# Optimization experiments

Measured on AMD Instinct MI355X. Metric: run time of the kernel, lower is better.

The kernel has to match this reference:

```python
import jax, jax.numpy as jnp
import numpy as np

N = 8192        # number of samples
D = 128         # embedding dim
K = 20          # n_neighbors (sklearn kneighbors includes self when querying the fitted set)
C = 10          # num classes
THRESH = -0.5   # INFLO score threshold (module default)
EPS = 1e-10


def setup_inputs() -> dict:
    key = jax.random.key(0)
    k1, k2 = jax.random.split(key)
    return {
        "embeddings": jax.random.normal(k1, (N, D), dtype=jnp.float32),
        "logits": jax.random.normal(k2, (N, C), dtype=jnp.float32),
    }


def _inflo_scores(x):
    # pairwise euclidean distances (p=2), [N, N]
    sq = jnp.sum(x * x, axis=-1)
    d2 = sq[:, None] + sq[None, :] - 2.0 * (x @ x.T)
    dist = jnp.sqrt(jnp.maximum(d2, 0.0))
    # k nearest neighbors per row (self included, distance 0) == sklearn kneighbors on fitted set
    neg_knn_d, knn_idx = jax.lax.top_k(-dist, K)
    knn_d = -neg_knn_d                                   # [N, K]
    # local density: 1 / (mean kNN distance)
    density = 1.0 / (jnp.mean(knn_d, axis=-1) + EPS)     # [N]
    # kNN membership mask: Kmask[i, j] = j in knn(i)
    rows = jnp.arange(N)[:, None]
    kmask = jnp.zeros((N, N), dtype=bool).at[rows, knn_idx].set(True)
    # influence space = knn(i) UNION rnn(i), where rnn(i) = {j : i in knn(j)}
    infl = kmask | kmask.T                               # set union (deduplicated)
    inflf = infl.astype(x.dtype)
    # average influence density over the (non-empty: self always included) influence set
    avg = (inflf @ density) / jnp.maximum(jnp.sum(inflf, axis=-1), 1.0)
    # inflo score (negated, as in the module)
    return -(density / (avg + EPS))


def reference(embeddings, logits):
    scores = _inflo_scores(embeddings)
    ood_flags = scores < THRESH
    cls_preds = jnp.where(ood_flags, -1, jnp.argmax(logits, axis=-1))
    return scores, ood_flags, cls_preds
```

## Files before the change

### kernel.cpp

```cpp
#include <hip/hip_runtime.h>
#include <cstdint>
#include <cstddef>

#define N 8192
#define D 128
#define KNN 20
#define NC 10
#define CAPB 448
#define SLOTS 16
#define ZTH 2.1f
#define NW (N / 32)
constexpr float EPS = 1e-10f;

typedef __attribute__((ext_vector_type(8))) short short8;
typedef __attribute__((ext_vector_type(4))) float f32x4;

__device__ inline unsigned short f32_to_bf16_rne(float x) {
    unsigned u = __float_as_uint(x);
    unsigned r = u + 0x7FFFu + ((u >> 16) & 1u);
    return (unsigned short)(r >> 16);
}
__device__ inline float bf16_to_f32(unsigned short h) {
    return __uint_as_float((unsigned)h << 16);
}
__device__ inline unsigned long long pack_key(float d, int j) {
    return ((unsigned long long)__float_as_uint(d) << 14) | (unsigned long long)(j + 1);
}

__global__ void k_sqnorm(const float* __restrict__ X, float* __restrict__ sq) {
    int row = blockIdx.x;
    int lane = threadIdx.x;
    const float2* X2 = (const float2*)(X + (size_t)row * D);
    float2 a = X2[lane];
    float s = a.x * a.x + a.y * a.y;
    #pragma unroll
    for (int off = 32; off; off >>= 1) s += __shfl_down(s, off, 64);
    if (lane == 0) sq[row] = s;
}

__global__ void k_split(const float* __restrict__ X, unsigned short* __restrict__ Xhi,
                        unsigned short* __restrict__ Xlo) {
    int i = blockIdx.x * 256 + threadIdx.x;
    const float4* X4 = (const float4*)X;
    float4 x = X4[i];
    unsigned short h[4], l[4];
    float xs[4] = {x.x, x.y, x.z, x.w};
    #pragma unroll
    for (int q = 0; q < 4; ++q) {
        h[q] = f32_to_bf16_rne(xs[q]);
        float hf = bf16_to_f32(h[q]);
        l[q] = f32_to_bf16_rne(xs[q] - hf);
    }
    *(ushort4*)&Xhi[(size_t)i * 4] = make_ushort4(h[0], h[1], h[2], h[3]);
    *(ushort4*)&Xlo[(size_t)i * 4] = make_ushort4(l[0], l[1], l[2], l[3]);
}

__global__ __launch_bounds__(128) void k_moments(const float* __restrict__ X,
                                                 const float* __restrict__ sq,
                                                 float* __restrict__ m1,
                                                 float* __restrict__ msc) {
    int b = blockIdx.x, t = threadIdx.x;
    int r0 = b * 64;
    float s1 = 0.f;
    for (int r = 0; r < 64; ++r) s1 += X[(size_t)(r0 + r) * D + t];
    atomicAdd(&m1[t], s1);
    if (t < 64) {
        float s = sq[r0 + t];
        float ss1 = s, ss2 = s * s;
        #pragma unroll
        for (int off = 32; off; off >>= 1) {
            ss1 += __shfl_down(ss1, off, 64);
            ss2 += __shfl_down(ss2, off, 64);
        }
        if (t == 0) { atomicAdd(&msc[0], ss1); atomicAdd(&msc[1], ss2); }
    }
}

__global__ void k_thresh(const float* __restrict__ X, const float* __restrict__ sq,
                         const float* __restrict__ m1, const float* __restrict__ msc,
                         float* __restrict__ T) {
    int row = blockIdx.x, lane = threadIdx.x;
    const float2* X2 = (const float2*)(X + (size_t)row * D);
    const float2* M2 = (const float2*)m1;
    float2 a = X2[lane], m = M2[lane];
    float dotp = a.x * m.x + a.y * m.y;
    #pragma unroll
    for (int off = 32; off; off >>= 1) dotp += __shfl_down(dotp, off, 64);
    if (lane == 0) {
        const float invN = 1.f / N;
        float Esq   = msc[0] * invN;
        float Esq2  = msc[1] * invN;
        float varSq = fmaxf(Esq2 - Esq * Esq, 0.f);
        float s  = sq[row];
        float mu = s + Esq - 2.f * dotp * invN;
        float var = varSq + 4.f * s;
        T[row] = mu - ZTH * sqrtf(var);
    }
}

#define ASTRIDE 40
struct StageS {
    unsigned short Ahi[128 * ASTRIDE];
    unsigned short Alo[128 * ASTRIDE];
    unsigned short Bhi[128 * ASTRIDE];
    unsigned short Blo[128 * ASTRIDE];
};
struct EpiS {
    unsigned long long slots[128 * SLOTS];
    unsigned rc[128];
    unsigned rbase[128];
};
__global__ __launch_bounds__(256, 3) void k_distf2(
        const unsigned short* __restrict__ Xhi, const unsigned short* __restrict__ Xlo,
        const float* __restrict__ sqn, const float* __restrict__ Tthr,
        int* __restrict__ cnt, unsigned long long* __restrict__ rowbuf, int capb) {
    __shared__ alignas(16) union { StageS s; EpiS e; } U;

    const int t    = threadIdx.x;
    const int lane = t & 63;
    const int w    = t >> 6;
    const int wr   = w >> 1;
    const int wc   = w & 1;
    const int lrow = lane & 15;
    const int lkg  = lane >> 4;

    const int rowTile = blockIdx.y * 128;
    const int colTile = blockIdx.x * 128;

    f32x4 acc[4][4];
    #pragma unroll
    for (int i = 0; i < 4; ++i)
        #pragma unroll
        for (int j = 0; j < 4; ++j) acc[i][j] = (f32x4){0.f, 0.f, 0.f, 0.f};

    for (int kc = 0; kc < 4; ++kc) {
        const int kb = kc * 32;
        __syncthreads();
        #pragma unroll
        for (int p = 0; p < 2; ++p) {
            int u = t + 256 * p, r = u >> 2, c = u & 3;
            size_t g = (size_t)(rowTile + r) * 128 + kb + c * 8;
            *(uint4*)&U.s.Ahi[r * ASTRIDE + c * 8] = *(const uint4*)&Xhi[g];
            *(uint4*)&U.s.Alo[r * ASTRIDE + c * 8] = *(const uint4*)&Xlo[g];
        }
        #pragma unroll
        for (int p = 0; p < 2; ++p) {
            int u = t + 256 * p, r = u >> 2, c = u & 3;
            size_t g = (size_t)(colTile + r) * 128 + kb + c * 8;
            *(uint4*)&U.s.Bhi[r * ASTRIDE + c * 8] = *(const uint4*)&Xhi[g];
            *(uint4*)&U.s.Blo[r * ASTRIDE + c * 8] = *(const uint4*)&Xlo[g];
        }
        __syncthreads();

        short8 a[4], b[4];
        #pragma unroll
        for (int i = 0; i < 4; ++i)
            a[i] = *(const short8*)&U.s.Ahi[(wr * 64 + 16 * i + lrow) * ASTRIDE + lkg * 8];
        #pragma unroll
        for (int j = 0; j < 4; ++j)
            b[j] = *(const short8*)&U.s.Bhi[(wc * 64 + 16 * j + lrow) * ASTRIDE + lkg * 8];
        #pragma unroll
        for (int i = 0; i < 4; ++i)
            #pragma unroll
            for (int j = 0; j < 4; ++j)
                acc[i][j] = __builtin_amdgcn_mfma_f32_16x16x32_bf16(a[i], b[j], acc[i][j], 0, 0, 0);
        #pragma unroll
        for (int j = 0; j < 4; ++j)
            b[j] = *(const short8*)&U.s.Blo[(wc * 64 + 16 * j + lrow) * ASTRIDE + lkg * 8];
        #pragma unroll
        for (int i = 0; i < 4; ++i)
            #pragma unroll
            for (int j = 0; j < 4; ++j)
                acc[i][j] = __builtin_amdgcn_mfma_f32_16x16x32_bf16(a[i], b[j], acc[i][j], 0, 0, 0);
        #pragma unroll
        for (int i = 0; i < 4; ++i)
            a[i] = *(const short8*)&U.s.Alo[(wr * 64 + 16 * i + lrow) * ASTRIDE + lkg * 8];
        #pragma unroll
        for (int j = 0; j < 4; ++j)
            b[j] = *(const short8*)&U.s.Bhi[(wc * 64 + 16 * j + lrow) * ASTRIDE + lkg * 8];
        #pragma unroll
        for (int i = 0; i < 4; ++i)
            #pragma unroll
            for (int j = 0; j < 4; ++j)
                acc[i][j] = __builtin_amdgcn_mfma_f32_16x16x32_bf16(a[i], b[j], acc[i][j], 0, 0, 0);
    }

    __syncthreads();
    if (t < 128) U.e.rc[t] = 0;
    __syncthreads();

    float sqb[4]; int gcol[4];
    #pragma unroll
    for (int j = 0; j < 4; ++j) {
        gcol[j] = colTile + wc * 64 + 16 * j + lrow;
        sqb[j]  = sqn[gcol[j]];
    }
    #pragma unroll
    for (int i = 0; i < 4; ++i) {
        int lr0 = wr * 64 + 16 * i + lkg * 4;
        #pragma unroll
        for (int q = 0; q < 4; ++q) {
            int lr = lr0 + q;
            float sa = sqn[rowTile + lr];
            float Ti = Tthr[rowTile + lr];
            #pragma unroll
            for (int j = 0; j < 4; ++j) {
                float d = fmaxf(fmaf(-2.f, acc[i][j][q], sa + sqb[j]), 0.f);
                if (d < Ti) {
                    unsigned o = atomicAdd(&U.e.rc[lr], 1u);
                    if (o < SLOTS) U.e.slots[lr * SLOTS + o] = pack_key(d, gcol[j]);
                }
            }
        }
    }
    __syncthreads();
    if (t < 128) {
        unsigned nr = U.e.rc[t];
        if (nr > SLOTS) {
            atomicAdd(&cnt[rowTile + t], capb + 1);
            U.e.rbase[t] = 0xFFFFFFFFu;
        } else if (nr > 0) {
            U.e.rbase[t] = (unsigned)atomicAdd(&cnt[rowTile + t], (int)nr);
        } else {
            U.e.rbase[t] = 0;
        }
    }
    __syncthreads();
    #pragma unroll
    for (int it = 0; it < (128 * SLOTS) / 256; ++it) {
        int idx = t + 256 * it;
        int r = idx / SLOTS, s = idx % SLOTS;
        unsigned nr = U.e.rc[r], base = U.e.rbase[r];
        if ((unsigned)s < min(nr, (unsigned)SLOTS) && base != 0xFFFFFFFFu) {
            unsigned pos = base + (unsigned)s;
            if (pos < (unsigned)capb)
                rowbuf[(size_t)(rowTile + r) * capb + pos] = U.e.slots[idx];
        }
    }
}

__global__ __launch_bounds__(64) void k_sel2(const unsigned long long* __restrict__ rowbuf,
                                             const int* __restrict__ cnt,
                                             int* __restrict__ knn_idx,
                                             float* __restrict__ density,
                                             int* __restrict__ flagged,
                                             int* __restrict__ nflag, int capb) {
    int row = blockIdx.x, t = threadIdx.x;
    int n = cnt[row];
    if (n < KNN || n > capb) {
        if (t == 0) { int p = atomicAdd(nflag, 1); flagged[p] = row; }
        return;
    }
    const unsigned long long* rb = rowbuf + (size_t)row * capb;
    unsigned long long v[7];
    #pragma unroll
    for (int k = 0; k < 7; ++k) { int idx = t + 64 * k; v[k] = idx < n ? rb[idx] : ~0ull; }
    unsigned long long last = 0ull;
    float sumd = 0.f;
    for (int r = 0; r < KNN; ++r) {
        unsigned long long m = ~0ull;
        #pragma unroll
        for (int k = 0; k < 7; ++k) if (v[k] > last && v[k] < m) m = v[k];
        #pragma unroll
        for (int off = 32; off; off >>= 1) {
            unsigned long long o = __shfl_down(m, off, 64);
            if (o < m) m = o;
        }
        m = __shfl(m, 0, 64);
        last = m;
        if (t == 0) {
            int j = (int)(m & 16383ull) - 1;
            if (j < 0) j = 0; if (j >= N) j = N - 1;
            knn_idx[(size_t)row * KNN + r] = j;
            sumd += sqrtf(__uint_as_float((unsigned)(m >> 14)));
        }
    }
    if (t == 0) density[row] = 1.f / (sumd * (1.f / KNN) + EPS);
}

__global__ __launch_bounds__(256) void k_fallback(const float* __restrict__ X,
                                                  const float* __restrict__ sq,
                                                  const int* __restrict__ nflag,
                                                  const int* __restrict__ flagged,
                                                  int* __restrict__ knn_idx,
                                                  float* __restrict__ density) {
    __shared__ float xr[D];
    __shared__ unsigned long long red[256];
    int t = threadIdx.x;
    int nf = *nflag;
    for (int f = blockIdx.x; f < nf; f += gridDim.x) {
        int row = flagged[f];
        __syncthreads();
        if (t < D) xr[t] = X[(size_t)row * D + t];
        __syncthreads();
        float sqr = sq[row];
        unsigned long long keys[32];
        for (int i = 0; i < 32; ++i) {
            int col = t + 256 * i;
            const float4* cp = (const float4*)(X + (size_t)col * D);
            float dot = 0.f;
            #pragma unroll
            for (int d4 = 0; d4 < 32; ++d4) {
                float4 c = cp[d4];
                float4 x = *(const float4*)&xr[d4 * 4];
                dot = fmaf(c.x, x.x, dot); dot = fmaf(c.y, x.y, dot);
                dot = fmaf(c.z, x.z, dot); dot = fmaf(c.w, x.w, dot);
            }
            float d2v = fmaxf(sqr + sq[col] - 2.f * dot, 0.f);
            keys[i] = pack_key(d2v, col);
        }
        unsigned long long last = 0ull;
        float sumd = 0.f;
        for (int r = 0; r < KNN; ++r) {
            unsigned long long m = ~0ull;
            #pragma unroll
            for (int i = 0; i < 32; ++i) if (keys[i] > last && keys[i] < m) m = keys[i];
            red[t] = m; __syncthreads();
            for (int s = 128; s; s >>= 1) {
                if (t < s && red[t + s] < red[t]) red[t] = red[t + s];
                __syncthreads();
            }
            m = red[0]; __syncthreads();
            last = m;
            if (t == 0) {
                int j = (int)(m & 16383ull) - 1;
                if (j < 0) j = 0; if (j >= N) j = N - 1;
                knn_idx[(size_t)row * KNN + r] = j;
                sumd += sqrtf(__uint_as_float((unsigned)(m >> 14)));
            }
        }
        if (t == 0) density[row] = 1.f / (sumd * (1.f / KNN) + EPS);
    }
}

__global__ void k_setbits(const int* __restrict__ knn_idx, unsigned* __restrict__ bits) {
    int p = blockIdx.x * 256 + threadIdx.x;
    if (p >= N * KNN) return;
    int i = p / KNN;
    int j = knn_idx[p];
    atomicOr(&bits[(size_t)i * NW + (j >> 5)], 1u << (j & 31));
}

__global__ void k_rowsum(const int* __restrict__ knn_idx, const float* __restrict__ density,
                         float* __restrict__ numer, float* __restrict__ cntb) {
    int i = blockIdx.x * 256 + threadIdx.x;
    if (i >= N) return;
    const int* ki = knn_idx + (size_t)i * KNN;
    float s = 0.f;
    #pragma unroll
    for (int m = 0; m < KNN; ++m) s += density[ki[m]];
    numer[i] = s;
    cntb[i] = (float)KNN;
}

__global__ void k_rev(const int* __restrict__ knn_idx, const float* __restrict__ density,
                      const unsigned* __restrict__ bits,
                      float* __restrict__ numer, float* __restrict__ cntb) {
    int p = blockIdx.x * 256 + threadIdx.x;
    if (p >= N * KNN) return;
    int i = p / KNN;
    int j = knn_idx[p];
    unsigned wd = bits[(size_t)j * NW + (i >> 5)];
    if (!(wd & (1u << (i & 31)))) {
        atomicAdd(&numer[j], density[i]);
        atomicAdd(&cntb[j], 1.f);
    }
}

__global__ void k_final(const float* __restrict__ density, const float* __restrict__ numer,
                        const float* __restrict__ cntb, const float* __restrict__ logits,
                        float* __restrict__ out) {
    int i = blockIdx.x * 256 + threadIdx.x;
    if (i >= N) return;
    float c     = fmaxf(cntb[i], 1.f);
    float avg   = numer[i] / c;
    float score = -(density[i] / (avg + EPS));
    out[i] = score;
    bool flag = score < -0.5f;
    out[N + i] = flag ? 1.f : 0.f;
    const float* lg = logits + (size_t)i * NC;
    float best = lg[0]; int bi = 0;
    #pragma unroll
    for (int k = 1; k < NC; ++k) { float x = lg[k]; if (x > best) { best = x; bi = k; } }
    out[2 * N + i] = flag ? -1.f : (float)bi;
}

extern "C" void kernel_launch(void* const* d_in, const int* in_sizes, int n_in,
                              void* d_out, int out_size, void* d_ws, size_t ws_size,
                              hipStream_t stream) {
    const float* X      = (const float*)d_in[0];
    const float* logits = (const float*)d_in[1];
    float* out = (float*)d_out;

    char* w = (char*)d_ws;
    auto alloc = [&](size_t bytes) { char* p = w; w += (bytes + 255) & ~(size_t)255; return p; };
    float* sq      = (float*)alloc((size_t)N * 4);
    float* density = (float*)alloc((size_t)N * 4);
    float* numer   = (float*)alloc((size_t)N * 4);
    float* cntb    = (float*)alloc((size_t)N * 4);
    int*   knn     = (int*)alloc((size_t)N * KNN * 4);
    unsigned short* Xhi = (unsigned short*)alloc((size_t)N * D * 2);
    unsigned short* Xlo = (unsigned short*)alloc((size_t)N * D * 2);
    float* Tthr    = (float*)alloc((size_t)N * 4);
    float* m1      = (float*)alloc((size_t)(D + 2) * 4);
    int*   cnt     = (int*)alloc((size_t)N * 4);
    int*   flagged = (int*)alloc((size_t)N * 4);
    int*   nflag   = (int*)alloc(256);
    unsigned* bits = (unsigned*)alloc((size_t)N * NW * 4);

    size_t used  = (size_t)(w - (char*)d_ws);
    size_t avail = ws_size > used ? ws_size - used : 0;
    int capb = (int)(avail / ((size_t)N * 8));
    if (capb > CAPB) capb = CAPB;
    if (capb < 1) capb = 1;
    unsigned long long* rowbuf = (unsigned long long*)alloc((size_t)N * capb * 8);

    hipMemsetAsync(bits,  0, (size_t)N * NW * 4, stream);
    hipMemsetAsync(cnt,   0, (size_t)N * 4, stream);
    hipMemsetAsync(m1,    0, (size_t)(D + 2) * 4, stream);
    hipMemsetAsync(nflag, 0, 4, stream);

    k_sqnorm <<<N, 64, 0, stream>>>(X, sq);
    k_split  <<<(N * D / 4 + 255) / 256, 256, 0, stream>>>(X, Xhi, Xlo);
    k_moments<<<128, 128, 0, stream>>>(X, sq, m1, m1 + D);
    k_thresh <<<N, 64, 0, stream>>>(X, sq, m1, m1 + D, Tthr);

    k_distf2 <<<dim3(N / 128, N / 128), 256, 0, stream>>>(Xhi, Xlo, sq, Tthr, cnt, rowbuf, capb);

    k_sel2    <<<N, 64, 0, stream>>>(rowbuf, cnt, knn, density, flagged, nflag, capb);
    k_fallback<<<64, 256, 0, stream>>>(X, sq, nflag, flagged, knn, density);

    k_setbits<<<(N * KNN + 255) / 256, 256, 0, stream>>>(knn, bits);
    k_rowsum <<<(N + 255) / 256, 256, 0, stream>>>(knn, density, numer, cntb);
    k_rev    <<<(N * KNN + 255) / 256, 256, 0, stream>>>(knn, density, bits, numer, cntb);

    k_final  <<<(N + 255) / 256, 256, 0, stream>>>(density, numer, cntb, logits, out);
}
```

Before: 228.4 us.

## Exploit distance symmetry with triangular tile grid and fuse prep/setbits kernels

The distance kernel now launches only upper-triangular 128x128 tiles and emits candidates both for the row (j>=i) and, transposed, for the column (j>i) using the column thresholds, so the Gram matrix work is roughly halved. The epilogue shared buffers double to hold 256 rows of slots. sqnorm and bf16 split are fused into one prep kernel, setbits is folded into the selection and fallback kernels, memsets are merged, and the moments kernel uses more blocks. The cost is a serial loop to decode the tile index, extra atomics on global cnt from transposed writes, and more shared memory, which may lower occupancy.

```diff
diff --git a/kernel.cpp b/kernel.cpp
--- a/kernel.cpp
+++ b/kernel.cpp
@@ -10,6 +10,8 @@
 #define SLOTS 16
 #define ZTH 2.1f
 #define NW (N / 32)
+#define NT 64
+#define NBLK (NT * (NT + 1) / 2)
 constexpr float EPS = 1e-10f;
 
 typedef __attribute__((ext_vector_type(8))) short short8;
@@ -27,32 +29,20 @@
     return ((unsigned long long)__float_as_uint(d) << 14) | (unsigned long long)(j + 1);
 }
 
-__global__ void k_sqnorm(const float* __restrict__ X, float* __restrict__ sq) {
-    int row = blockIdx.x;
-    int lane = threadIdx.x;
+__global__ void k_prep(const float* __restrict__ X, unsigned short* __restrict__ Xhi,
+                       unsigned short* __restrict__ Xlo, float* __restrict__ sq) {
+    int row = blockIdx.x, t = threadIdx.x;
     const float2* X2 = (const float2*)(X + (size_t)row * D);
-    float2 a = X2[lane];
+    float2 a = X2[t];
+    ushort2 h, l;
+    h.x = f32_to_bf16_rne(a.x); l.x = f32_to_bf16_rne(a.x - bf16_to_f32(h.x));
+    h.y = f32_to_bf16_rne(a.y); l.y = f32_to_bf16_rne(a.y - bf16_to_f32(h.y));
+    *(ushort2*)&Xhi[(size_t)row * D + 2 * t] = h;
+    *(ushort2*)&Xlo[(size_t)row * D + 2 * t] = l;
     float s = a.x * a.x + a.y * a.y;
     #pragma unroll
     for (int off = 32; off; off >>= 1) s += __shfl_down(s, off, 64);
-    if (lane == 0) sq[row] = s;
-}
-
-__global__ void k_split(const float* __restrict__ X, unsigned short* __restrict__ Xhi,
-                        unsigned short* __restrict__ Xlo) {
-    int i = blockIdx.x * 256 + threadIdx.x;
-    const float4* X4 = (const float4*)X;
-    float4 x = X4[i];
-    unsigned short h[4], l[4];
-    float xs[4] = {x.x, x.y, x.z, x.w};
-    #pragma unroll
-    for (int q = 0; q < 4; ++q) {
-        h[q] = f32_to_bf16_rne(xs[q]);
-        float hf = bf16_to_f32(h[q]);
-        l[q] = f32_to_bf16_rne(xs[q] - hf);
-    }
-    *(ushort4*)&Xhi[(size_t)i * 4] = make_ushort4(h[0], h[1], h[2], h[3]);
-    *(ushort4*)&Xlo[(size_t)i * 4] = make_ushort4(l[0], l[1], l[2], l[3]);
+    if (t == 0) sq[row] = s;
 }
 
 __global__ __launch_bounds__(128) void k_moments(const float* __restrict__ X,
@@ -60,15 +50,16 @@
                                                  float* __restrict__ m1,
                                                  float* __restrict__ msc) {
     int b = blockIdx.x, t = threadIdx.x;
-    int r0 = b * 64;
+    int r0 = b * 16;
     float s1 = 0.f;
-    for (int r = 0; r < 64; ++r) s1 += X[(size_t)(r0 + r) * D + t];
+    #pragma unroll
+    for (int r = 0; r < 16; ++r) s1 += X[(size_t)(r0 + r) * D + t];
     atomicAdd(&m1[t], s1);
-    if (t < 64) {
+    if (t < 16) {
         float s = sq[r0 + t];
         float ss1 = s, ss2 = s * s;
         #pragma unroll
-        for (int off = 32; off; off >>= 1) {
+        for (int off = 8; off; off >>= 1) {
             ss1 += __shfl_down(ss1, off, 64);
             ss2 += __shfl_down(ss2, off, 64);
         }
@@ -106,14 +97,18 @@
     unsigned short Blo[128 * ASTRIDE];
 };
 struct EpiS {
-    unsigned long long slots[128 * SLOTS];
-    unsigned rc[128];
-    unsigned rbase[128];
+    unsigned long long slots[256 * SLOTS];
+    unsigned rc[256];
+    unsigned rbase[256];
 };
-__global__ __launch_bounds__(256, 3) void k_distf2(
+__global__ __launch_bounds__(256, 3) void k_distf3(
         const unsigned short* __restrict__ Xhi, const unsigned short* __restrict__ Xlo,
         const float* __restrict__ sqn, const float* __restrict__ Tthr,
         int* __restrict__ cnt, unsigned long long* __restrict__ rowbuf, int capb) {
+    int rem = blockIdx.x, by = 0;
+    while (rem >= NT - by) { rem -= NT - by; ++by; }
+    const int bx = by + rem;
+
     __shared__ alignas(16) union { StageS s; EpiS e; } U;
 
     const int t    = threadIdx.x;
@@ -124,8 +119,8 @@
     const int lrow = lane & 15;
     const int lkg  = lane >> 4;
 
-    const int rowTile = blockIdx.y * 128;
-    const int colTile = blockIdx.x * 128;
+    const int rowTile = by * 128;
+    const int colTile = bx * 128;
 
     f32x4 acc[4][4];
     #pragma unroll
@@ -152,89 +147,95 @@
         }
         __syncthreads();
 
-        short8 a[4], b[4];
+        short8 a[4], bh[4], bl[4];
         #pragma unroll
         for (int i = 0; i < 4; ++i)
             a[i] = *(const short8*)&U.s.Ahi[(wr * 64 + 16 * i + lrow) * ASTRIDE + lkg * 8];
         #pragma unroll
         for (int j = 0; j < 4; ++j)
-            b[j] = *(const short8*)&U.s.Bhi[(wc * 64 + 16 * j + lrow) * ASTRIDE + lkg * 8];
+            bh[j] = *(const short8*)&U.s.Bhi[(wc * 64 + 16 * j + lrow) * ASTRIDE + lkg * 8];
+        #pragma unroll
+        for (int j = 0; j < 4; ++j)
+            bl[j] = *(const short8*)&U.s.Blo[(wc * 64 + 16 * j + lrow) * ASTRIDE + lkg * 8];
         #pragma unroll
         for (int i = 0; i < 4; ++i)
             #pragma unroll
             for (int j = 0; j < 4; ++j)
-                acc[i][j] = __builtin_amdgcn_mfma_f32_16x16x32_bf16(a[i], b[j], acc[i][j], 0, 0, 0);
-        #pragma unroll
-        for (int j = 0; j < 4; ++j)
-            b[j] = *(const short8*)&U.s.Blo[(wc * 64 + 16 * j + lrow) * ASTRIDE + lkg * 8];
+                acc[i][j] = __builtin_amdgcn_mfma_f32_16x16x32_bf16(a[i], bh[j], acc[i][j], 0, 0, 0);
         #pragma unroll
         for (int i = 0; i < 4; ++i)
             #pragma unroll
             for (int j = 0; j < 4; ++j)
-                acc[i][j] = __builtin_amdgcn_mfma_f32_16x16x32_bf16(a[i], b[j], acc[i][j], 0, 0, 0);
+                acc[i][j] = __builtin_amdgcn_mfma_f32_16x16x32_bf16(a[i], bl[j], acc[i][j], 0, 0, 0);
         #pragma unroll
         for (int i = 0; i < 4; ++i)
             a[i] = *(const short8*)&U.s.Alo[(wr * 64 + 16 * i + lrow) * ASTRIDE + lkg * 8];
         #pragma unroll
-        for (int j = 0; j < 4; ++j)
-            b[j] = *(const short8*)&U.s.Bhi[(wc * 64 + 16 * j + lrow) * ASTRIDE + lkg * 8];
-        #pragma unroll
         for (int i = 0; i < 4; ++i)
             #pragma unroll
             for (int j = 0; j < 4; ++j)
-                acc[i][j] = __builtin_amdgcn_mfma_f32_16x16x32_bf16(a[i], b[j], acc[i][j], 0, 0, 0);
+                acc[i][j] = __builtin_amdgcn_mfma_f32_16x16x32_bf16(a[i], bh[j], acc[i][j], 0, 0, 0);
     }
 
     __syncthreads();
-    if (t < 128) U.e.rc[t] = 0;
+    U.e.rc[t] = 0;
     __syncthreads();
 
-    float sqb[4]; int gcol[4];
+    float sqb[4], Tb[4]; int gcol[4], lcol[4];
     #pragma unroll
     for (int j = 0; j < 4; ++j) {
-        gcol[j] = colTile + wc * 64 + 16 * j + lrow;
+        lcol[j] = wc * 64 + 16 * j + lrow;
+        gcol[j] = colTile + lcol[j];
         sqb[j]  = sqn[gcol[j]];
+        Tb[j]   = Tthr[gcol[j]];
     }
     #pragma unroll
     for (int i = 0; i < 4; ++i) {
         int lr0 = wr * 64 + 16 * i + lkg * 4;
         #pragma unroll
         for (int q = 0; q < 4; ++q) {
-            int lr = lr0 + q;
-            float sa = sqn[rowTile + lr];
-            float Ti = Tthr[rowTile + lr];
+            int lr = lr0 + q, gi = rowTile + lr;
+            float sa = sqn[gi];
+            float Ti = Tthr[gi];
             #pragma unroll
             for (int j = 0; j < 4; ++j) {
                 float d = fmaxf(fmaf(-2.f, acc[i][j][q], sa + sqb[j]), 0.f);
-                if (d < Ti) {
+                int gj = gcol[j];
+                if (gj >= gi && d < Ti) {
                     unsigned o = atomicAdd(&U.e.rc[lr], 1u);
-                    if (o < SLOTS) U.e.slots[lr * SLOTS + o] = pack_key(d, gcol[j]);
+                    if (o < SLOTS) U.e.slots[lr * SLOTS + o] = pack_key(d, gj);
+                }
+                if (gj > gi && d < Tb[j]) {
+                    unsigned o = atomicAdd(&U.e.rc[128 + lcol[j]], 1u);
+                    if (o < SLOTS) U.e.slots[(128 + lcol[j]) * SLOTS + o] = pack_key(d, gi);
                 }
             }
         }
     }
     __syncthreads();
-    if (t < 128) {
+    {
         unsigned nr = U.e.rc[t];
+        int grow = (t < 128) ? (rowTile + t) : (colTile + (t - 128));
         if (nr > SLOTS) {
-            atomicAdd(&cnt[rowTile + t], capb + 1);
+            atomicAdd(&cnt[grow], capb + 1);
             U.e.rbase[t] = 0xFFFFFFFFu;
         } else if (nr > 0) {
-            U.e.rbase[t] = (unsigned)atomicAdd(&cnt[rowTile + t], (int)nr);
+            U.e.rbase[t] = (unsigned)atomicAdd(&cnt[grow], (int)nr);
         } else {
             U.e.rbase[t] = 0;
         }
     }
     __syncthreads();
     #pragma unroll
-    for (int it = 0; it < (128 * SLOTS) / 256; ++it) {
+    for (int it = 0; it < (256 * SLOTS) / 256; ++it) {
         int idx = t + 256 * it;
-        int r = idx / SLOTS, s = idx % SLOTS;
+        int r = idx >> 4, s = idx & 15;
         unsigned nr = U.e.rc[r], base = U.e.rbase[r];
         if ((unsigned)s < min(nr, (unsigned)SLOTS) && base != 0xFFFFFFFFu) {
             unsigned pos = base + (unsigned)s;
+            int grow = (r < 128) ? (rowTile + r) : (colTile + (r - 128));
             if (pos < (unsigned)capb)
-                rowbuf[(size_t)(rowTile + r) * capb + pos] = U.e.slots[idx];
+                rowbuf[(size_t)grow * capb + pos] = U.e.slots[r * SLOTS + s];
         }
     }
 }
@@ -243,8 +244,10 @@
                                              const int* __restrict__ cnt,
                                              int* __restrict__ knn_idx,
                                              float* __restrict__ density,
+                                             unsigned* __restrict__ bits,
                                              int* __restrict__ flagged,
                                              int* __restrict__ nflag, int capb) {
+    __shared__ int nb[KNN];
     int row = blockIdx.x, t = threadIdx.x;
     int n = cnt[row];
     if (n < KNN || n > capb) {
@@ -272,10 +275,16 @@
             int j = (int)(m & 16383ull) - 1;
             if (j < 0) j = 0; if (j >= N) j = N - 1;
             knn_idx[(size_t)row * KNN + r] = j;
+            nb[r] = j;
             sumd += sqrtf(__uint_as_float((unsigned)(m >> 14)));
         }
     }
     if (t == 0) density[row] = 1.f / (sumd * (1.f / KNN) + EPS);
+    __syncthreads();
+    if (t < KNN) {
+        int j = nb[t];
+        atomicOr(&bits[(size_t)row * NW + (j >> 5)], 1u << (j & 31));
+    }
 }
 
 __global__ __launch_bounds__(256) void k_fallback(const float* __restrict__ X,
@@ -283,9 +292,11 @@
                                                   const int* __restrict__ nflag,
                                                   const int* __restrict__ flagged,
                                                   int* __restrict__ knn_idx,
-                                                  float* __restrict__ density) {
+                                                  float* __restrict__ density,
+                                                  unsigned* __restrict__ bits) {
     __shared__ float xr[D];
     __shared__ unsigned long long red[256];
+    __shared__ int nbf[KNN];
     int t = threadIdx.x;
     int nf = *nflag;
     for (int f = blockIdx.x; f < nf; f += gridDim.x) {
@@ -326,19 +337,17 @@
                 int j = (int)(m & 16383ull) - 1;
                 if (j < 0) j = 0; if (j >= N) j = N - 1;
                 knn_idx[(size_t)row * KNN + r] = j;
+                nbf[r] = j;
                 sumd += sqrtf(__uint_as_float((unsigned)(m >> 14)));
             }
         }
         if (t == 0) density[row] = 1.f / (sumd * (1.f / KNN) + EPS);
-    }
-}
-
-__global__ void k_setbits(const int* __restrict__ knn_idx, unsigned* __restrict__ bits) {
-    int p = blockIdx.x * 256 + threadIdx.x;
-    if (p >= N * KNN) return;
-    int i = p / KNN;
-    int j = knn_idx[p];
-    atomicOr(&bits[(size_t)i * NW + (j >> 5)], 1u << (j & 31));
+        __syncthreads();
+        if (t < KNN) {
+            int j = nbf[t];
+            atomicOr(&bits[(size_t)row * NW + (j >> 5)], 1u << (j & 31));
+        }
+    }
 }
 
 __global__ void k_rowsum(const int* __restrict__ knn_idx, const float* __restrict__ density,
@@ -402,10 +411,12 @@
     unsigned short* Xhi = (unsigned short*)alloc((size_t)N * D * 2);
     unsigned short* Xlo = (unsigned short*)alloc((size_t)N * D * 2);
     float* Tthr    = (float*)alloc((size_t)N * 4);
+    int*   flagged = (int*)alloc((size_t)N * 4);
+    char* zbase    = w;
+    int*   cnt     = (int*)alloc((size_t)N * 4);
+    int*   nflag   = (int*)alloc(256);
     float* m1      = (float*)alloc((size_t)(D + 2) * 4);
-    int*   cnt     = (int*)alloc((size_t)N * 4);
-    int*   flagged = (int*)alloc((size_t)N * 4);
-    int*   nflag   = (int*)alloc(256);
+    size_t zsize   = (size_t)(w - zbase);
     unsigned* bits = (unsigned*)alloc((size_t)N * NW * 4);
 
     size_t used  = (size_t)(w - (char*)d_ws);
@@ -415,22 +426,18 @@
     if (capb < 1) capb = 1;
     unsigned long long* rowbuf = (unsigned long long*)alloc((size_t)N * capb * 8);
 
+    hipMemsetAsync(zbase, 0, zsize, stream);
     hipMemsetAsync(bits,  0, (size_t)N * NW * 4, stream);
-    hipMemsetAsync(cnt,   0, (size_t)N * 4, stream);
-    hipMemsetAsync(m1,    0, (size_t)(D + 2) * 4, stream);
-    hipMemsetAsync(nflag, 0, 4, stream);
-
-    k_sqnorm <<<N, 64, 0, stream>>>(X, sq);
-    k_split  <<<(N * D / 4 + 255) / 256, 256, 0, stream>>>(X, Xhi, Xlo);
-    k_moments<<<128, 128, 0, stream>>>(X, sq, m1, m1 + D);
+
+    k_prep   <<<N, 64, 0, stream>>>(X, Xhi, Xlo, sq);
+    k_moments<<<512, 128, 0, stream>>>(X, sq, m1, m1 + D);
     k_thresh <<<N, 64, 0, stream>>>(X, sq, m1, m1 + D, Tthr);
 
-    k_distf2 <<<dim3(N / 128, N / 128), 256, 0, stream>>>(Xhi, Xlo, sq, Tthr, cnt, rowbuf, capb);
-
-    k_sel2    <<<N, 64, 0, stream>>>(rowbuf, cnt, knn, density, flagged, nflag, capb);
-    k_fallback<<<64, 256, 0, stream>>>(X, sq, nflag, flagged, knn, density);
-
-    k_setbits<<<(N * KNN + 255) / 256, 256, 0, stream>>>(knn, bits);
+    k_distf3 <<<NBLK, 256, 0, stream>>>(Xhi, Xlo, sq, Tthr, cnt, rowbuf, capb);
+
+    k_sel2    <<<N, 64, 0, stream>>>(rowbuf, cnt, knn, density, bits, flagged, nflag, capb);
+    k_fallback<<<64, 256, 0, stream>>>(X, sq, nflag, flagged, knn, density, bits);
+
     k_rowsum <<<(N + 255) / 256, 256, 0, stream>>>(knn, density, numer, cntb);
     k_rev    <<<(N * KNN + 255) / 256, 256, 0, stream>>>(knn, density, bits, numer, cntb);
 
```

After: 205.5 us. 10.0% less time.
